# Performance work log

Hardware: AMD Instinct MI355X
Metric: run time of the kernel (lower is better)

## Reference

```python
import jax, jax.numpy as jnp
import numpy as np

Z, N, K, W = 131072, 64, 64, 32


def setup_inputs() -> dict:
    key = jax.random.key(0)
    k1, k2, k3 = jax.random.split(key, 3)
    features = jax.random.normal(k1, (Z, N), dtype=jnp.float32)
    # dense realization of the CG-derived mixing tensor 'wkij'
    mixing_matrix = jax.random.normal(k2, (W, K, N, N), dtype=jnp.float32) * 0.05
    weight = jax.random.normal(k3, (W,), dtype=jnp.float32)
    return {"features": features, "mixing_matrix": mixing_matrix, "weight": weight}


def reference(features, mixing_matrix, weight):
    # torch: einsum('w,wkij,zi,zj->zk', weight, mixing_matrix, features, features)
    # Contract the small path axis w first -> [K, N, N] (cheap, tiny output),
    # then the bilinear square over z. einsum chooses a GEMM-style path; the
    # [Z, N, N] outer-product side is the memory-bound part.
    M = jnp.einsum('w,wkij->kij', weight, mixing_matrix)  # [K, N, N]
    out = jnp.einsum('kij,zi,zj->zk', M, features, features)  # [Z, K]
    return out
```

## Files before the change

### kernel.cpp

```cpp
#include <hip/hip_runtime.h>
#include <stdint.h>

typedef __attribute__((ext_vector_type(8))) short short8;
typedef __attribute__((ext_vector_type(4))) float f32x4;

#define NCHUNK 64
#define BROWS  72
#define XD     65

__device__ __forceinline__ unsigned short f2bf_rne(float f) {
  unsigned u = __builtin_bit_cast(unsigned, f);
  u += 0x7fffu + ((u >> 16) & 1u);
  return (unsigned short)(u >> 16);
}
__device__ __forceinline__ float bf2f(unsigned short s) {
  unsigned u = ((unsigned)s) << 16;
  return __builtin_bit_cast(float, u);
}
__device__ __forceinline__ unsigned pack_bf2(float p0, float p1) {
  return __builtin_amdgcn_perm(__builtin_bit_cast(unsigned, p1),
                               __builtin_bit_cast(unsigned, p0), 0x07060302u);
}

__global__ __launch_bounds__(256) void prep_kernel(const float* __restrict__ mix,
                                                   const float* __restrict__ wgt,
                                                   unsigned short* __restrict__ Bp) {
  __shared__ float4 red[256];
  const int tid = threadIdx.x;
  const int ws  = tid >> 6;
  const int tt  = tid & 63;
  const int t4  = blockIdx.x * 64 + tt;
  const float4* m4 = (const float4*)mix;
  float ax = 0.f, ay = 0.f, az = 0.f, aw = 0.f;
#pragma unroll
  for (int wi = 0; wi < 8; ++wi) {
    const int w = ws * 8 + wi;
    const float s = wgt[w];
    const float4 v = m4[w * 65536 + t4];
    ax += s * v.x; ay += s * v.y; az += s * v.z; aw += s * v.w;
  }
  red[tid] = (float4){ax, ay, az, aw};
  __syncthreads();
  if (tid < 64) {
    const float4 a = red[tid], b = red[tid + 64], c = red[tid + 128], d = red[tid + 192];
    ushort4 r;
    r.x = f2bf_rne(a.x + b.x + c.x + d.x);
    r.y = f2bf_rne(a.y + b.y + c.y + d.y);
    r.z = f2bf_rne(a.z + b.z + c.z + d.z);
    r.w = f2bf_rne(a.w + b.w + c.w + d.w);
    ((ushort4*)Bp)[blockIdx.x * 64 + tid] = r;
  }
}

__global__ __launch_bounds__(128, 2) void gemm_kernel(const float* __restrict__ X,
                                                      const unsigned short* __restrict__ Bp,
                                                      float* __restrict__ out) {
  __shared__ unsigned short ldsB[2][64 * BROWS];
  __shared__ unsigned ldsX[64 * XD];

  const int tid  = threadIdx.x;
  const int lane = tid & 63;
  const int wv   = tid >> 6;
  const int m    = lane & 15;
  const int q    = lane >> 4;
  const int zblk = blockIdx.x * 128;

  {
    const float4* X4 = (const float4*)(X + (size_t)zblk * 64);
#pragma unroll
    for (int it = 0; it < 8; ++it) {
      const int lin = tid + it * 128;
      const int zz  = lin >> 4;
      const int c4  = lin & 15;
      const float4 v0 = X4[(2 * zz) * 16 + c4];
      const float4 v1 = X4[(2 * zz + 1) * 16 + c4];
      float a0[4], a1[4];
      *(float4*)a0 = v0; *(float4*)a1 = v1;
#pragma unroll
      for (int r = 0; r < 4; ++r) {
        const unsigned pk = (unsigned)f2bf_rne(a0[r]) | ((unsigned)f2bf_rne(a1[r]) << 16);
        ldsX[(c4 * 4 + r) * XD + zz] = pk;
      }
    }
  }
  {
#pragma unroll
    for (int it = 0; it < 4; ++it) {
      const int lin = tid + it * 128;
      const int row = lin >> 3;
      const int cc  = lin & 7;
      const uint4 v = *(const uint4*)(Bp + row * 4096 + cc * 8);
      *(uint4*)(&ldsB[0][row * BROWS + cc * 8]) = v;
    }
  }

  float jv[4][16];
  {
    const float4* X4g = (const float4*)X;
#pragma unroll
    for (int f = 0; f < 4; ++f) {
      const int zg = zblk + wv * 64 + f * 16 + m;
#pragma unroll
      for (int h = 0; h < 2; ++h) {
        const float4 a = X4g[zg * 16 + h * 8 + q * 2];
        const float4 b = X4g[zg * 16 + h * 8 + q * 2 + 1];
        jv[f][h*8+0]=a.x; jv[f][h*8+1]=a.y; jv[f][h*8+2]=a.z; jv[f][h*8+3]=a.w;
        jv[f][h*8+4]=b.x; jv[f][h*8+5]=b.y; jv[f][h*8+6]=b.z; jv[f][h*8+7]=b.w;
      }
    }
  }

  f32x4 acc[4][4];
#pragma unroll
  for (int f = 0; f < 4; ++f)
#pragma unroll
    for (int g = 0; g < 4; ++g) acc[f][g] = f32x4{0.f, 0.f, 0.f, 0.f};

  __syncthreads();

  const unsigned short* xs = (const unsigned short*)ldsX;

  for (int c = 0; c < NCHUNK; ++c) {
    uint4 pre[4];
    const int cn = (c + 1) & (NCHUNK - 1);
#pragma unroll
    for (int it = 0; it < 4; ++it) {
      const int lin = tid + it * 128;
      const int row = lin >> 3;
      const int cc  = lin & 7;
      pre[it] = *(const uint4*)(Bp + row * 4096 + cn * 64 + cc * 8);
    }

    float s[4];
#pragma unroll
    for (int f = 0; f < 4; ++f)
      s[f] = bf2f(xs[c * (2 * XD) + wv * 64 + f * 16 + m]);

    const unsigned short* Bl = ldsB[c & 1];
#pragma unroll
    for (int h = 0; h < 2; ++h) {
      const unsigned short* bb = Bl + m * BROWS + h * 32 + q * 8;
      const short8 b0 = *(const short8*)(bb);
      const short8 b1 = *(const short8*)(bb + 16 * BROWS);
      const short8 b2 = *(const short8*)(bb + 32 * BROWS);
      const short8 b3 = *(const short8*)(bb + 48 * BROWS);
#pragma unroll
      for (int f = 0; f < 4; ++f) {
        union { unsigned u[4]; short8 v; } A;
#pragma unroll
        for (int e = 0; e < 4; ++e)
          A.u[e] = pack_bf2(s[f] * jv[f][h * 8 + 2 * e], s[f] * jv[f][h * 8 + 2 * e + 1]);
        acc[f][0] = __builtin_amdgcn_mfma_f32_16x16x32_bf16(A.v, b0, acc[f][0], 0, 0, 0);
        acc[f][1] = __builtin_amdgcn_mfma_f32_16x16x32_bf16(A.v, b1, acc[f][1], 0, 0, 0);
        acc[f][2] = __builtin_amdgcn_mfma_f32_16x16x32_bf16(A.v, b2, acc[f][2], 0, 0, 0);
        acc[f][3] = __builtin_amdgcn_mfma_f32_16x16x32_bf16(A.v, b3, acc[f][3], 0, 0, 0);
      }
    }

    {
      unsigned short* dst = ldsB[(c + 1) & 1];
#pragma unroll
      for (int it = 0; it < 4; ++it) {
        const int lin = tid + it * 128;
        const int row = lin >> 3;
        const int cc  = lin & 7;
        *(uint4*)(&dst[row * BROWS + cc * 8]) = pre[it];
      }
    }
    __syncthreads();
  }

#pragma unroll
  for (int f = 0; f < 4; ++f) {
    const int zr = zblk + wv * 64 + f * 16 + q * 4;
#pragma unroll
    for (int g = 0; g < 4; ++g)
#pragma unroll
      for (int r = 0; r < 4; ++r)
        out[(size_t)(zr + r) * 64 + g * 16 + m] = acc[f][g][r];
  }
}

extern "C" void kernel_launch(void* const* d_in, const int* in_sizes, int n_in,
                              void* d_out, int out_size, void* d_ws, size_t ws_size,
                              hipStream_t stream) {
  const float* X   = (const float*)d_in[0];
  const float* mix = (const float*)d_in[1];
  const float* wgt = (const float*)d_in[2];
  float* out = (float*)d_out;
  unsigned short* Bp = (unsigned short*)d_ws;

  prep_kernel<<<1024, 256, 0, stream>>>(mix, wgt, Bp);
  gemm_kernel<<<1024, 128, 0, stream>>>(X, Bp, out);
}
```

Measured before the change: 164.5 us.

## Double the z tile per block and process two i-slices per chunk

```diff
diff --git a/kernel.cpp b/kernel.cpp
--- a/kernel.cpp
+++ b/kernel.cpp
@@ -3,19 +3,16 @@
 
 typedef __attribute__((ext_vector_type(8))) short short8;
 typedef __attribute__((ext_vector_type(4))) float f32x4;
-
-#define NCHUNK 64
-#define BROWS  72
-#define XD     65
+typedef __attribute__((ext_vector_type(2))) float v2f;
+
+#define NCHUNK 32
+#define BROWS  136
+#define XROWD  132
 
 __device__ __forceinline__ unsigned short f2bf_rne(float f) {
   unsigned u = __builtin_bit_cast(unsigned, f);
   u += 0x7fffu + ((u >> 16) & 1u);
   return (unsigned short)(u >> 16);
-}
-__device__ __forceinline__ float bf2f(unsigned short s) {
-  unsigned u = ((unsigned)s) << 16;
-  return __builtin_bit_cast(float, u);
 }
 __device__ __forceinline__ unsigned pack_bf2(float p0, float p1) {
   return __builtin_amdgcn_perm(__builtin_bit_cast(unsigned, p1),
@@ -52,118 +49,136 @@
   }
 }
 
-__global__ __launch_bounds__(128, 2) void gemm_kernel(const float* __restrict__ X,
+__global__ __launch_bounds__(128, 1) void gemm_kernel(const float* __restrict__ X,
                                                       const unsigned short* __restrict__ Bp,
                                                       float* __restrict__ out) {
   __shared__ unsigned short ldsB[2][64 * BROWS];
-  __shared__ unsigned ldsX[64 * XD];
+  __shared__ unsigned ldsX[64 * XROWD];
 
   const int tid  = threadIdx.x;
   const int lane = tid & 63;
   const int wv   = tid >> 6;
   const int m    = lane & 15;
   const int q    = lane >> 4;
-  const int zblk = blockIdx.x * 128;
+  const int zblk = blockIdx.x * 256;
 
   {
     const float4* X4 = (const float4*)(X + (size_t)zblk * 64);
+    const int rr   = tid & 63;
+    const int ms   = (rr >> 2) & 15;
+    const int f2   = rr & 3;
+    const int ze   = wv * 128 + f2 * 32 + ms;
+    const int zo   = ze + 16;
+    const int dcol = wv * 64 + ms * 4 + f2;
+#pragma unroll 4
+    for (int c4 = 0; c4 < 16; ++c4) {
+      const float4 ve = X4[ze * 16 + c4];
+      const float4 vo = X4[zo * 16 + c4];
+      float ae[4], ao[4];
+      *(float4*)ae = ve; *(float4*)ao = vo;
+#pragma unroll
+      for (int r = 0; r < 4; ++r) {
+        const unsigned pk = (unsigned)f2bf_rne(ae[r]) | ((unsigned)f2bf_rne(ao[r]) << 16);
+        ldsX[(c4 * 4 + r) * XROWD + dcol] = pk;
+      }
+    }
+  }
+  {
 #pragma unroll
     for (int it = 0; it < 8; ++it) {
       const int lin = tid + it * 128;
-      const int zz  = lin >> 4;
-      const int c4  = lin & 15;
-      const float4 v0 = X4[(2 * zz) * 16 + c4];
-      const float4 v1 = X4[(2 * zz + 1) * 16 + c4];
-      float a0[4], a1[4];
-      *(float4*)a0 = v0; *(float4*)a1 = v1;
-#pragma unroll
-      for (int r = 0; r < 4; ++r) {
-        const unsigned pk = (unsigned)f2bf_rne(a0[r]) | ((unsigned)f2bf_rne(a1[r]) << 16);
-        ldsX[(c4 * 4 + r) * XD + zz] = pk;
-      }
-    }
-  }
-  {
-#pragma unroll
-    for (int it = 0; it < 4; ++it) {
-      const int lin = tid + it * 128;
-      const int row = lin >> 3;
-      const int cc  = lin & 7;
+      const int row = lin >> 4;
+      const int cc  = lin & 15;
       const uint4 v = *(const uint4*)(Bp + row * 4096 + cc * 8);
       *(uint4*)(&ldsB[0][row * BROWS + cc * 8]) = v;
     }
   }
 
-  float jv[4][16];
+  v2f jv2[8][8];
   {
     const float4* X4g = (const float4*)X;
 #pragma unroll
-    for (int f = 0; f < 4; ++f) {
-      const int zg = zblk + wv * 64 + f * 16 + m;
+    for (int f = 0; f < 8; ++f) {
+      const int zg = zblk + wv * 128 + f * 16 + m;
 #pragma unroll
       for (int h = 0; h < 2; ++h) {
         const float4 a = X4g[zg * 16 + h * 8 + q * 2];
         const float4 b = X4g[zg * 16 + h * 8 + q * 2 + 1];
-        jv[f][h*8+0]=a.x; jv[f][h*8+1]=a.y; jv[f][h*8+2]=a.z; jv[f][h*8+3]=a.w;
-        jv[f][h*8+4]=b.x; jv[f][h*8+5]=b.y; jv[f][h*8+6]=b.z; jv[f][h*8+7]=b.w;
-      }
-    }
-  }
-
-  f32x4 acc[4][4];
-#pragma unroll
-  for (int f = 0; f < 4; ++f)
+        jv2[f][h * 4 + 0] = v2f{a.x, a.y};
+        jv2[f][h * 4 + 1] = v2f{a.z, a.w};
+        jv2[f][h * 4 + 2] = v2f{b.x, b.y};
+        jv2[f][h * 4 + 3] = v2f{b.z, b.w};
+      }
+    }
+  }
+
+  f32x4 acc[8][4];
+#pragma unroll
+  for (int f = 0; f < 8; ++f)
 #pragma unroll
     for (int g = 0; g < 4; ++g) acc[f][g] = f32x4{0.f, 0.f, 0.f, 0.f};
 
   __syncthreads();
 
-  const unsigned short* xs = (const unsigned short*)ldsX;
-
   for (int c = 0; c < NCHUNK; ++c) {
-    uint4 pre[4];
+    uint4 pre[8];
     const int cn = (c + 1) & (NCHUNK - 1);
 #pragma unroll
-    for (int it = 0; it < 4; ++it) {
+    for (int it = 0; it < 8; ++it) {
       const int lin = tid + it * 128;
-      const int row = lin >> 3;
-      const int cc  = lin & 7;
-      pre[it] = *(const uint4*)(Bp + row * 4096 + cn * 64 + cc * 8);
-    }
-
-    float s[4];
-#pragma unroll
-    for (int f = 0; f < 4; ++f)
-      s[f] = bf2f(xs[c * (2 * XD) + wv * 64 + f * 16 + m]);
+      const int row = lin >> 4;
+      const int cc  = lin & 15;
+      pre[it] = *(const uint4*)(Bp + row * 4096 + cn * 128 + cc * 8);
+    }
 
     const unsigned short* Bl = ldsB[c & 1];
-#pragma unroll
-    for (int h = 0; h < 2; ++h) {
-      const unsigned short* bb = Bl + m * BROWS + h * 32 + q * 8;
-      const short8 b0 = *(const short8*)(bb);
-      const short8 b1 = *(const short8*)(bb + 16 * BROWS);
-      const short8 b2 = *(const short8*)(bb + 32 * BROWS);
-      const short8 b3 = *(const short8*)(bb + 48 * BROWS);
-#pragma unroll
-      for (int f = 0; f < 4; ++f) {
-        union { unsigned u[4]; short8 v; } A;
-#pragma unroll
-        for (int e = 0; e < 4; ++e)
-          A.u[e] = pack_bf2(s[f] * jv[f][h * 8 + 2 * e], s[f] * jv[f][h * 8 + 2 * e + 1]);
-        acc[f][0] = __builtin_amdgcn_mfma_f32_16x16x32_bf16(A.v, b0, acc[f][0], 0, 0, 0);
-        acc[f][1] = __builtin_amdgcn_mfma_f32_16x16x32_bf16(A.v, b1, acc[f][1], 0, 0, 0);
-        acc[f][2] = __builtin_amdgcn_mfma_f32_16x16x32_bf16(A.v, b2, acc[f][2], 0, 0, 0);
-        acc[f][3] = __builtin_amdgcn_mfma_f32_16x16x32_bf16(A.v, b3, acc[f][3], 0, 0, 0);
+    const unsigned* xs = ldsX;
+
+#pragma unroll
+    for (int il = 0; il < 2; ++il) {
+      const int i = c * 2 + il;
+      const uint4 sv4 = *(const uint4*)(xs + i * XROWD + wv * 64 + m * 4);
+      float sf[8];
+      {
+        unsigned d[4];
+        *(uint4*)d = sv4;
+#pragma unroll
+        for (int j = 0; j < 4; ++j) {
+          sf[2 * j]     = __builtin_bit_cast(float, d[j] << 16);
+          sf[2 * j + 1] = __builtin_bit_cast(float, d[j] & 0xffff0000u);
+        }
+      }
+#pragma unroll
+      for (int h = 0; h < 2; ++h) {
+        const unsigned short* bb = Bl + m * BROWS + il * 64 + h * 32 + q * 8;
+        const short8 b0 = *(const short8*)(bb);
+        const short8 b1 = *(const short8*)(bb + 16 * BROWS);
+        const short8 b2 = *(const short8*)(bb + 32 * BROWS);
+        const short8 b3 = *(const short8*)(bb + 48 * BROWS);
+#pragma unroll
+        for (int f = 0; f < 8; ++f) {
+          const v2f s2 = v2f{sf[f], sf[f]};
+          union { unsigned u[4]; short8 v; } A;
+#pragma unroll
+          for (int e = 0; e < 4; ++e) {
+            const v2f pr = s2 * jv2[f][h * 4 + e];
+            A.u[e] = pack_bf2(pr[0], pr[1]);
+          }
+          acc[f][0] = __builtin_amdgcn_mfma_f32_16x16x32_bf16(A.v, b0, acc[f][0], 0, 0, 0);
+          acc[f][1] = __builtin_amdgcn_mfma_f32_16x16x32_bf16(A.v, b1, acc[f][1], 0, 0, 0);
+          acc[f][2] = __builtin_amdgcn_mfma_f32_16x16x32_bf16(A.v, b2, acc[f][2], 0, 0, 0);
+          acc[f][3] = __builtin_amdgcn_mfma_f32_16x16x32_bf16(A.v, b3, acc[f][3], 0, 0, 0);
+        }
       }
     }
 
     {
       unsigned short* dst = ldsB[(c + 1) & 1];
 #pragma unroll
-      for (int it = 0; it < 4; ++it) {
+      for (int it = 0; it < 8; ++it) {
         const int lin = tid + it * 128;
-        const int row = lin >> 3;
-        const int cc  = lin & 7;
+        const int row = lin >> 4;
+        const int cc  = lin & 15;
         *(uint4*)(&dst[row * BROWS + cc * 8]) = pre[it];
       }
     }
@@ -171,8 +186,8 @@
   }
 
 #pragma unroll
-  for (int f = 0; f < 4; ++f) {
-    const int zr = zblk + wv * 64 + f * 16 + q * 4;
+  for (int f = 0; f < 8; ++f) {
+    const int zr = zblk + wv * 128 + f * 16 + q * 4;
 #pragma unroll
     for (int g = 0; g < 4; ++g)
 #pragma unroll
@@ -191,5 +206,5 @@
   unsigned short* Bp = (unsigned short*)d_ws;
 
   prep_kernel<<<1024, 256, 0, stream>>>(mix, wgt, Bp);
-  gemm_kernel<<<1024, 128, 0, stream>>>(X, Bp, out);
-}
+  gemm_kernel<<<512, 128, 0, stream>>>(X, Bp, out);
+}
```

Result: slower. 245.5 us (+49.2%).
